# Kernel tuning notes

Measured on AMD Instinct MI355X. Metric: run time of the kernel, lower is better.

Reference implementation:

```python
import jax, jax.numpy as jnp
import numpy as np

CROSS_SIZES = [256, 256, 256]  # split_half=True -> carried field sizes [39,128,128,256]


def setup_inputs() -> dict:
    key = jax.random.key(0)
    ks = jax.random.split(key, 6)
    B, F, D = 1024, 39, 32
    scale = 0.05
    return {
        "x": jax.random.normal(ks[0], (B, F, D), dtype=jnp.float32),
        "W0": jax.random.normal(ks[1], (F * F, 256), dtype=jnp.float32) * scale,
        "b0": jnp.zeros((256,), dtype=jnp.float32),
        "W1": jax.random.normal(ks[2], (F * 128, 256), dtype=jnp.float32) * scale,
        "b1": jnp.zeros((256,), dtype=jnp.float32),
        "W2": jax.random.normal(ks[3], (F * 128, 256), dtype=jnp.float32) * scale,
        "b2": jnp.zeros((256,), dtype=jnp.float32),
        "fc_w": jax.random.normal(ks[4], (512, 1), dtype=jnp.float32) * scale,
        "fc_b": jnp.zeros((1,), dtype=jnp.float32),
    }


def reference(x, W0, b0, W1, b1, W2, b2, fc_w, fc_b):
    # x: (B, F, D)
    B, F, D = x.shape
    params = [(W0, b0), (W1, b1), (W2, b2)]
    n_layers = len(params)
    x0 = x
    h = x            # carried state, (B, Hi, D)
    finals = []
    for i, (W, b) in enumerate(params):
        Hp = h.shape[1]
        # per-embedding-dim outer product of fields, flattened: (B, D, F*Hp)
        z = jnp.einsum('bfd,bhd->bdfh', x0, h).reshape(B, D, F * Hp)
        # conv1d with kernel width 1 == dense projection over the F*Hp axis
        out = jax.nn.relu(z @ W + b)          # (B, D, O)
        out = jnp.transpose(out, (0, 2, 1))   # (B, O, D)
        if i != n_layers - 1:
            half = CROSS_SIZES[i] // 2
            h = out[:, :half]        # next_tmp (first half)
            finals.append(out[:, half:])  # h (second half)
        else:
            finals.append(out)
    res = jnp.concatenate(finals, axis=1)  # (B, 512, D)
    res = jnp.sum(res, axis=-1)            # (B, 512)
    return res @ fc_w + fc_b               # (B, 1)
```

## Files before the change

### kernel.cpp

```cpp
#include <hip/hip_runtime.h>
#include <stdint.h>


typedef unsigned int u32;
typedef unsigned short u16;
typedef __attribute__((ext_vector_type(8))) unsigned short us8;
typedef __attribute__((ext_vector_type(8))) _Float16 half8;
typedef __attribute__((ext_vector_type(4))) float f32x4;

__device__ __forceinline__ u16 f32_to_f16u(float f) {
  union { _Float16 h; u16 u; } c;
  c.h = (_Float16)f;
  return c.u;
}
__device__ __forceinline__ u32 pkmul(u32 a, u32 b) {
  u32 r;
  asm("v_pk_mul_f16 %0, %1, %2" : "=v"(r) : "v"(a), "v"(b));
  return r;
}
__device__ __forceinline__ void gload16(const u16* g, u16* l) {
  __builtin_amdgcn_global_load_lds((const __attribute__((address_space(1))) u32*)g,
                                   (__attribute__((address_space(3))) u32*)l, 16, 0, 0);
}
__device__ __forceinline__ void wait_vm4() {
  asm volatile("s_waitcnt vmcnt(4)" ::: "memory");
  __builtin_amdgcn_sched_barrier(0);
}
__device__ __forceinline__ void wait_vm0() {
  asm volatile("s_waitcnt vmcnt(0)" ::: "memory");
  __builtin_amdgcn_sched_barrier(0);
}

__global__ void prep_wt(const float* __restrict__ W0, const float* __restrict__ W1,
                        const float* __restrict__ W2, u16* __restrict__ WT0,
                        u16* __restrict__ WT1, u16* __restrict__ WT2) {
  int blk = blockIdx.x;
  const float* W;
  u16* WT;
  int KPAD, kp0;
  bool l0 = false;
  if (blk < 312) { W = W0; WT = WT0; KPAD = 2496; kp0 = blk * 8; l0 = true; }
  else if (blk < 936) { W = W1; WT = WT1; KPAD = 4992; kp0 = (blk - 312) * 8; }
  else { W = W2; WT = WT2; KPAD = 4992; kp0 = (blk - 936) * 8; }

  __shared__ u16 lds[8][257];
  int t = threadIdx.x;
  #pragma unroll
  for (int kk = 0; kk < 8; ++kk) {
    int kp = kp0 + kk;
    float v;
    if (l0) {
      int f = kp >> 6, hh = kp & 63;
      v = (hh < 39) ? W[(f * 39 + hh) * 256 + t] : 0.f;
    } else {
      v = W[kp * 256 + t];
    }
    lds[kk][t] = f32_to_f16u(v);
  }
  __syncthreads();
  us8 o;
  #pragma unroll
  for (int kk = 0; kk < 8; ++kk) o[kk] = lds[kk][t];
  *(us8*)(&WT[(size_t)t * KPAD + kp0]) = o;
}

template <int LAYER>
__global__ __launch_bounds__(512, 4) void cin_layer(
    const float* __restrict__ x, const u16* __restrict__ hin,
    const u16* __restrict__ WT, const float* __restrict__ bias,
    u16* __restrict__ hout, float* __restrict__ fsum) {
  constexpr int HPAD = (LAYER == 0) ? 64 : 128;
  constexpr int KPAD = 39 * HPAD;
  constexpr int HC2 = HPAD / 64;
  constexpr int NT = 39 * HC2;

  __shared__ __align__(16) u16 wtile[2][256 * 64];
  __shared__ u32 x0pk[2][32][41];

  const int tid = threadIdx.x;
  const int bbase = blockIdx.x * 2;

  for (int idx = tid; idx < 2 * 1248; idx += 512) {
    int b = idx / 1248;
    int rem = idx - b * 1248;
    int f = rem >> 5, d = rem & 31;
    u16 xh = f32_to_f16u(x[(bbase + b) * 1248 + rem]);
    x0pk[b][d][f] = (u32)xh | ((u32)xh << 16);
  }

  const int lane = tid & 63;
  const int w = tid >> 6;
  const int l15 = lane & 15;
  const int g = lane >> 4;

  int rs[4], rd[4];
  #pragma unroll
  for (int m = 0; m < 4; ++m) {
    int row = m * 16 + l15;
    rs[m] = row >> 5;
    rd[m] = row & 31;
  }

  const int nloc = lane >> 3, slot = lane & 7;
  const int qq = slot ^ nloc;
  const u16* wsrc = WT + (size_t)(w * 32 + nloc) * KPAD + qq * 8;

  const int xorm = (l15 & 7) * 8;
  const int rB0 = (w * 32 + l15) * 64;

  f32x4 acc[4][2];
  #pragma unroll
  for (int m = 0; m < 4; ++m)
    #pragma unroll
    for (int n = 0; n < 2; ++n) acc[m][n] = (f32x4){0.f, 0.f, 0.f, 0.f};

  {
    u16* dst = &wtile[0][(w * 32) * 64];
    #pragma unroll
    for (int j = 0; j < 4; ++j) gload16(wsrc + (size_t)j * 8 * KPAD, dst + j * 8 * 64);
  }
  __syncthreads();

  union HF { u32 u[4]; half8 h; us8 s; };
  int tt = 0;
  for (int t = 0; t < HC2; ++t) {
    HF hf2[4][2];
    if (LAYER == 0) {
      #pragma unroll
      for (int m = 0; m < 4; ++m)
        #pragma unroll
        for (int c = 0; c < 2; ++c)
          #pragma unroll
          for (int i = 0; i < 4; ++i) {
            int h0 = c * 32 + g * 8 + 2 * i;
            u32 lo = (h0 < 39) ? (x0pk[rs[m]][rd[m]][h0] & 0xffffu) : 0u;
            u32 hi = (h0 + 1 < 39) ? (x0pk[rs[m]][rd[m]][h0 + 1] & 0xffffu) : 0u;
            hf2[m][c].u[i] = lo | (hi << 16);
          }
    } else {
      #pragma unroll
      for (int m = 0; m < 4; ++m)
        #pragma unroll
        for (int c = 0; c < 2; ++c)
          hf2[m][c].s = *(const us8*)(
              &hin[(((size_t)(bbase + rs[m]) * 32 + rd[m]) << 7) + (2 * t + c) * 32 + g * 8]);
    }
    for (int f = 0; f < 39; ++f, ++tt) {
      const int buf = tt & 1;
      const bool more = (tt + 1 < NT);
      if (more) {
        const int nf = (f + 1 < 39) ? f + 1 : 0;
        const int ntp = (f + 1 < 39) ? t : t + 1;
        const int koff = nf * HPAD + ntp * 64;
        u16* dst = &wtile[buf ^ 1][(w * 32) * 64];
        #pragma unroll
        for (int j = 0; j < 4; ++j)
          gload16(wsrc + (size_t)j * 8 * KPAD + koff, dst + j * 8 * 64);
        wait_vm4();
      } else {
        wait_vm0();
      }
      u32 xs[4];
      #pragma unroll
      for (int m = 0; m < 4; ++m) xs[m] = x0pk[rs[m]][rd[m]][f];
      #pragma unroll
      for (int c = 0; c < 2; ++c) {
        const int off = (c * 32 + g * 8) ^ xorm;
        HF b0, b1;
        b0.s = *(const us8*)(&wtile[buf][rB0 + off]);
        b1.s = *(const us8*)(&wtile[buf][rB0 + 16 * 64 + off]);
        #pragma unroll
        for (int m = 0; m < 4; ++m) {
          HF a;
          #pragma unroll
          for (int i = 0; i < 4; ++i) a.u[i] = pkmul(hf2[m][c].u[i], xs[m]);
          acc[m][0] = __builtin_amdgcn_mfma_f32_16x16x32_f16(a.h, b0.h, acc[m][0], 0, 0, 0);
          acc[m][1] = __builtin_amdgcn_mfma_f32_16x16x32_f16(a.h, b1.h, acc[m][1], 0, 0, 0);
        }
      }
    }
  }

  __syncthreads();

  float bv[2];
  #pragma unroll
  for (int nt = 0; nt < 2; ++nt) bv[nt] = bias[w * 32 + nt * 16 + l15];

  if (LAYER < 2 && w < 4) {
    #pragma unroll
    for (int m = 0; m < 4; ++m)
      #pragma unroll
      for (int nt = 0; nt < 2; ++nt) {
        int o = w * 32 + nt * 16 + l15;
        #pragma unroll
        for (int r = 0; r < 4; ++r) {
          int row = m * 16 + g * 4 + r;
          int s = row >> 5, d = row & 31;
          float v = fmaxf(acc[m][nt][r] + bv[nt], 0.f);
          hout[(((bbase + s) * 32 + d) << 7) + o] = f32_to_f16u(v);
        }
      }
  } else {
    #pragma unroll
    for (int nt = 0; nt < 2; ++nt) {
      float sub[2] = {0.f, 0.f};
      #pragma unroll
      for (int m = 0; m < 4; ++m)
        #pragma unroll
        for (int r = 0; r < 4; ++r)
          sub[m >> 1] += fmaxf(acc[m][nt][r] + bv[nt], 0.f);
      #pragma unroll
      for (int s = 0; s < 2; ++s) {
        sub[s] += __shfl_xor(sub[s], 16);
        sub[s] += __shfl_xor(sub[s], 32);
      }
      if (lane < 16) {
        int o = w * 32 + nt * 16 + l15;
        int j = (LAYER == 0) ? (o - 128) : ((LAYER == 1) ? o : (256 + o));
        fsum[(bbase + 0) * 512 + j] = sub[0];
        fsum[(bbase + 1) * 512 + j] = sub[1];
      }
    }
  }
}

__global__ void finalize(const float* __restrict__ fsum, const float* __restrict__ fc_w,
                         const float* __restrict__ fc_b, float* __restrict__ out) {
  int b = blockIdx.x;
  int lane = threadIdx.x;
  const float* fs = fsum + (size_t)b * 512;
  float s = 0.f;
  #pragma unroll
  for (int k = 0; k < 8; ++k) {
    int j = k * 64 + lane;
    s += fs[j] * fc_w[j];
  }
  #pragma unroll
  for (int off = 32; off; off >>= 1) s += __shfl_xor(s, off);
  if (lane == 0) out[b] = s + fc_b[0];
}

extern "C" void kernel_launch(void* const* d_in, const int* in_sizes, int n_in,
                              void* d_out, int out_size, void* d_ws, size_t ws_size,
                              hipStream_t stream) {
  const float* x = (const float*)d_in[0];
  const float* W0 = (const float*)d_in[1];
  const float* b0 = (const float*)d_in[2];
  const float* W1 = (const float*)d_in[3];
  const float* b1 = (const float*)d_in[4];
  const float* W2 = (const float*)d_in[5];
  const float* b2 = (const float*)d_in[6];
  const float* fc_w = (const float*)d_in[7];
  const float* fc_b = (const float*)d_in[8];
  float* out = (float*)d_out;

  char* ws = (char*)d_ws;
  size_t oWT0 = 0;
  size_t oWT1 = oWT0 + (size_t)256 * 2496 * 2;
  size_t oWT2 = oWT1 + (size_t)256 * 4992 * 2;
  size_t oH = oWT2 + (size_t)256 * 4992 * 2;
  size_t oFS = oH + (size_t)1024 * 32 * 128 * 2;
  u16* WT0 = (u16*)(ws + oWT0);
  u16* WT1 = (u16*)(ws + oWT1);
  u16* WT2 = (u16*)(ws + oWT2);
  u16* hbuf = (u16*)(ws + oH);
  float* fsum = (float*)(ws + oFS);

  prep_wt<<<1560, 256, 0, stream>>>(W0, W1, W2, WT0, WT1, WT2);
  cin_layer<0><<<512, 512, 0, stream>>>(x, nullptr, WT0, b0, hbuf, fsum);
  cin_layer<1><<<512, 512, 0, stream>>>(x, hbuf, WT1, b1, hbuf, fsum);
  cin_layer<2><<<512, 512, 0, stream>>>(x, hbuf, WT2, b2, nullptr, fsum);
  finalize<<<1024, 64, 0, stream>>>(fsum, fc_w, fc_b, out);
}
```

Baseline: 226.7 us.

## Load weight fragments directly from global into registers, dropping LDS staging

Removes the double-buffered LDS weight tile filled by global_load_lds. Each lane now reads its MFMA B fragments straight from global memory into registers, with a ping-pong register prefetch of the next tile. This frees 64KB of LDS per block, which could raise occupancy, and removes the vmcnt waits. The cost is uncoalesced 16-byte global loads per lane with no cross-wave sharing, and a serial dependency on global load latency.

After: 422.6 us. 1.86x slower.

```diff
diff --git a/kernel.cpp b/kernel.cpp
--- a/kernel.cpp
+++ b/kernel.cpp
@@ -17,18 +17,6 @@
   u32 r;
   asm("v_pk_mul_f16 %0, %1, %2" : "=v"(r) : "v"(a), "v"(b));
   return r;
-}
-__device__ __forceinline__ void gload16(const u16* g, u16* l) {
-  __builtin_amdgcn_global_load_lds((const __attribute__((address_space(1))) u32*)g,
-                                   (__attribute__((address_space(3))) u32*)l, 16, 0, 0);
-}
-__device__ __forceinline__ void wait_vm4() {
-  asm volatile("s_waitcnt vmcnt(4)" ::: "memory");
-  __builtin_amdgcn_sched_barrier(0);
-}
-__device__ __forceinline__ void wait_vm0() {
-  asm volatile("s_waitcnt vmcnt(0)" ::: "memory");
-  __builtin_amdgcn_sched_barrier(0);
 }
 
 __global__ void prep_wt(const float* __restrict__ W0, const float* __restrict__ W1,
@@ -74,7 +62,6 @@
   constexpr int HC2 = HPAD / 64;
   constexpr int NT = 39 * HC2;
 
-  __shared__ __align__(16) u16 wtile[2][256 * 64];
   __shared__ u32 x0pk[2][32][41];
 
   const int tid = threadIdx.x;
@@ -101,12 +88,8 @@
     rd[m] = row & 31;
   }
 
-  const int nloc = lane >> 3, slot = lane & 7;
-  const int qq = slot ^ nloc;
-  const u16* wsrc = WT + (size_t)(w * 32 + nloc) * KPAD + qq * 8;
-
-  const int xorm = (l15 & 7) * 8;
-  const int rB0 = (w * 32 + l15) * 64;
+  const u16* wp0 = WT + (size_t)(w * 32 + l15) * KPAD + g * 8;
+  const u16* wp1 = wp0 + (size_t)16 * KPAD;
 
   f32x4 acc[4][2];
   #pragma unroll
@@ -114,70 +97,88 @@
     #pragma unroll
     for (int n = 0; n < 2; ++n) acc[m][n] = (f32x4){0.f, 0.f, 0.f, 0.f};
 
-  {
-    u16* dst = &wtile[0][(w * 32) * 64];
-    #pragma unroll
-    for (int j = 0; j < 4; ++j) gload16(wsrc + (size_t)j * 8 * KPAD, dst + j * 8 * 64);
-  }
   __syncthreads();
 
   union HF { u32 u[4]; half8 h; us8 s; };
-  int tt = 0;
-  for (int t = 0; t < HC2; ++t) {
-    HF hf2[4][2];
-    if (LAYER == 0) {
-      #pragma unroll
-      for (int m = 0; m < 4; ++m)
-        #pragma unroll
-        for (int c = 0; c < 2; ++c)
-          #pragma unroll
-          for (int i = 0; i < 4; ++i) {
-            int h0 = c * 32 + g * 8 + 2 * i;
-            u32 lo = (h0 < 39) ? (x0pk[rs[m]][rd[m]][h0] & 0xffffu) : 0u;
-            u32 hi = (h0 + 1 < 39) ? (x0pk[rs[m]][rd[m]][h0 + 1] & 0xffffu) : 0u;
-            hf2[m][c].u[i] = lo | (hi << 16);
-          }
-    } else {
+  HF hf2[4][2];
+  if (LAYER == 0) {
+    #pragma unroll
+    for (int m = 0; m < 4; ++m)
+      #pragma unroll
+      for (int c = 0; c < 2; ++c)
+        #pragma unroll
+        for (int i = 0; i < 4; ++i) {
+          int h0 = c * 32 + g * 8 + 2 * i;
+          u32 lo = (h0 < 39) ? (x0pk[rs[m]][rd[m]][h0] & 0xffffu) : 0u;
+          u32 hi = (h0 + 1 < 39) ? (x0pk[rs[m]][rd[m]][h0 + 1] & 0xffffu) : 0u;
+          hf2[m][c].u[i] = lo | (hi << 16);
+        }
+  } else {
+    #pragma unroll
+    for (int m = 0; m < 4; ++m)
+      #pragma unroll
+      for (int c = 0; c < 2; ++c)
+        hf2[m][c].s = *(const us8*)(
+            &hin[(((size_t)(bbase + rs[m]) * 32 + rd[m]) << 7) + c * 32 + g * 8]);
+  }
+
+  HF frA[2][2], frB[2][2];
+  u32 xsA[4], xsB[4];
+  #pragma unroll
+  for (int c = 0; c < 2; ++c) {
+    frA[c][0].s = *(const us8*)(wp0 + c * 32);
+    frA[c][1].s = *(const us8*)(wp1 + c * 32);
+  }
+  #pragma unroll
+  for (int m = 0; m < 4; ++m) xsA[m] = x0pk[rs[m]][rd[m]][0];
+
+  int f = 0, hc = 0;
+  auto tile = [&](HF(&cur)[2][2], HF(&nxt)[2][2], u32(&cxs)[4], u32(&nxs)[4]) {
+    int nf = f + 1, nhc = hc;
+    if (nf == 39) { nf = 0; ++nhc; }
+    const bool more = (nhc < HC2);
+    if (more) {
+      const int koff = nf * HPAD + nhc * 64;
+      #pragma unroll
+      for (int c = 0; c < 2; ++c) {
+        nxt[c][0].s = *(const us8*)(wp0 + koff + c * 32);
+        nxt[c][1].s = *(const us8*)(wp1 + koff + c * 32);
+      }
+      #pragma unroll
+      for (int m = 0; m < 4; ++m) nxs[m] = x0pk[rs[m]][rd[m]][nf];
+    }
+    #pragma unroll
+    for (int c = 0; c < 2; ++c)
+      #pragma unroll
+      for (int m = 0; m < 4; ++m) {
+        HF a;
+        #pragma unroll
+        for (int i = 0; i < 4; ++i) a.u[i] = pkmul(hf2[m][c].u[i], cxs[m]);
+        acc[m][0] = __builtin_amdgcn_mfma_f32_16x16x32_f16(a.h, cur[c][0].h, acc[m][0], 0, 0, 0);
+        acc[m][1] = __builtin_amdgcn_mfma_f32_16x16x32_f16(a.h, cur[c][1].h, acc[m][1], 0, 0, 0);
+      }
+    if (LAYER != 0 && more && nhc != hc) {
       #pragma unroll
       for (int m = 0; m < 4; ++m)
         #pragma unroll
         for (int c = 0; c < 2; ++c)
           hf2[m][c].s = *(const us8*)(
-              &hin[(((size_t)(bbase + rs[m]) * 32 + rd[m]) << 7) + (2 * t + c) * 32 + g * 8]);
-    }
-    for (int f = 0; f < 39; ++f, ++tt) {
-      const int buf = tt & 1;
-      const bool more = (tt + 1 < NT);
-      if (more) {
-        const int nf = (f + 1 < 39) ? f + 1 : 0;
-        const int ntp = (f + 1 < 39) ? t : t + 1;
-        const int koff = nf * HPAD + ntp * 64;
-        u16* dst = &wtile[buf ^ 1][(w * 32) * 64];
-        #pragma unroll
-        for (int j = 0; j < 4; ++j)
-          gload16(wsrc + (size_t)j * 8 * KPAD + koff, dst + j * 8 * 64);
-        wait_vm4();
-      } else {
-        wait_vm0();
-      }
-      u32 xs[4];
-      #pragma unroll
-      for (int m = 0; m < 4; ++m) xs[m] = x0pk[rs[m]][rd[m]][f];
-      #pragma unroll
-      for (int c = 0; c < 2; ++c) {
-        const int off = (c * 32 + g * 8) ^ xorm;
-        HF b0, b1;
-        b0.s = *(const us8*)(&wtile[buf][rB0 + off]);
-        b1.s = *(const us8*)(&wtile[buf][rB0 + 16 * 64 + off]);
-        #pragma unroll
-        for (int m = 0; m < 4; ++m) {
-          HF a;
-          #pragma unroll
-          for (int i = 0; i < 4; ++i) a.u[i] = pkmul(hf2[m][c].u[i], xs[m]);
-          acc[m][0] = __builtin_amdgcn_mfma_f32_16x16x32_f16(a.h, b0.h, acc[m][0], 0, 0, 0);
-          acc[m][1] = __builtin_amdgcn_mfma_f32_16x16x32_f16(a.h, b1.h, acc[m][1], 0, 0, 0);
-        }
-      }
+              &hin[(((size_t)(bbase + rs[m]) * 32 + rd[m]) << 7) + (2 * nhc + c) * 32 + g * 8]);
+    }
+    f = nf;
+    hc = nhc;
+  };
+
+  if constexpr (NT % 2 == 1) {
+    tile(frA, frB, xsA, xsB);
+    for (int p = 0; p < NT / 2; ++p) {
+      tile(frB, frA, xsB, xsA);
+      tile(frA, frB, xsA, xsB);
+    }
+  } else {
+    for (int p = 0; p < NT / 2; ++p) {
+      tile(frA, frB, xsA, xsB);
+      tile(frB, frA, xsB, xsA);
     }
   }
 
```
